# Optimization experiments

Measured on AMD Instinct MI355X. Metric: run time of the kernel, lower is better.

The kernel has to match this reference:

```python
import jax, jax.numpy as jnp
import numpy as np

VEC, H, B, S = 768, 256, 64, 512


def setup_inputs() -> dict:
    key = jax.random.key(0)
    ks = jax.random.split(key, 8)
    sc = 0.02
    return {
        "output_1": jax.random.normal(ks[0], (B, S, VEC), dtype=jnp.float32),
        "output_2": jax.random.normal(ks[1], (B, S, VEC), dtype=jnp.float32),
        "mlp_w": jax.random.normal(ks[2], (H, VEC), dtype=jnp.float32) * sc,
        "mlp_b": jnp.zeros((H,), dtype=jnp.float32),
        "fd_w": jax.random.normal(ks[3], (H, 2 * H), dtype=jnp.float32) * sc,
        "fd_b": jnp.zeros((H,), dtype=jnp.float32),
        "ff_w": jax.random.normal(ks[4], (1, H), dtype=jnp.float32) * sc,
        "ff_b": jnp.zeros((1,), dtype=jnp.float32),
    }


def reference(output_1, output_2, mlp_w, mlp_b, fd_w, fd_b, ff_w, ff_b):
    # eval-mode forward of Bert_coss
    o1 = jax.nn.relu(output_1 @ mlp_w.T + mlp_b)        # [B,S,H]
    o2 = jax.nn.relu(output_2 @ mlp_w.T + mlp_b)        # [B,S,H]
    o1_doc = jnp.mean(o1, axis=1)                        # [B,H]
    o2_doc = jnp.mean(o2, axis=1)                        # [B,H]
    h = jax.nn.relu(jnp.concatenate([o1_doc, o2_doc], axis=1) @ fd_w.T + fd_b)
    out = jax.nn.sigmoid(jnp.squeeze(h @ ff_w.T + ff_b))  # [B]
    # append doc vectors as an extra token
    o1e = jnp.concatenate([o1, o1_doc[:, None, :]], axis=1)  # [B,S+1,H]
    o2e = jnp.concatenate([o2, o2_doc[:, None, :]], axis=1)  # [B,S+1,H]
    # graph_match: scores + softmax over dim=1; only last column is used downstream
    a = jnp.einsum('bsh,bth->bst', o1e, o2e)             # [B,S+1,S+1]
    a_x = jax.nn.softmax(a, axis=1)
    att = a_x[:, :, -1].T                                # [S+1,B]
    att = jnp.concatenate([att[:-1], out[None, :]], axis=0)  # [S+1,B]
    return att
```

## Files before the change

### kernel.cpp

```cpp
#include <hip/hip_runtime.h>
#include <hip/hip_bf16.h>
#include <math.h>

#define B_ 64
#define S_ 512
#define VEC_ 768
#define H_ 256
#define M_ (B_*S_)

typedef float floatx4 __attribute__((ext_vector_type(4)));
typedef __bf16 bf16x8 __attribute__((ext_vector_type(8)));
typedef __bf16 bf16x4 __attribute__((ext_vector_type(4)));

__global__ __launch_bounds__(256) void prep_kernel(
    const float* __restrict__ mlp_w, __bf16* __restrict__ wbf, float* __restrict__ sums)
{
  const int bid = blockIdx.x;
  if (bid < 192) {
    const int i = bid * 256 + threadIdx.x;
    const float4 v = ((const float4*)mlp_w)[i];
    bf16x4 b = { (__bf16)v.x, (__bf16)v.y, (__bf16)v.z, (__bf16)v.w };
    *(bf16x4*)&wbf[(size_t)i * 4] = b;
  } else {
    const int i = (bid - 192) * 256 + threadIdx.x;
    ((float4*)sums)[i] = make_float4(0.f, 0.f, 0.f, 0.f);
  }
}

#define BUFSZ_ 16384
#define LDSB_  32768

__device__ __forceinline__ bf16x8 cvt8(float4 a, float4 b) {
  bf16x8 v;
  v[0] = (__bf16)a.x; v[1] = (__bf16)a.y; v[2] = (__bf16)a.z; v[3] = (__bf16)a.w;
  v[4] = (__bf16)b.x; v[5] = (__bf16)b.y; v[6] = (__bf16)b.z; v[7] = (__bf16)b.w;
  return v;
}

#define LOADT(A0, A1, A2, A3, Bv0, Bv1, kk)                                   \
  {                                                                           \
    const float*  pA_ = Aload + (kk);                                         \
    const __bf16* pB_ = Bload + (kk);                                         \
    A0 = *(const float4*)pA_;                                                 \
    A1 = *(const float4*)(pA_ + 4);                                           \
    A2 = *(const float4*)(pA_ + 64 * VEC_);                                   \
    A3 = *(const float4*)(pA_ + 64 * VEC_ + 4);                               \
    Bv0 = *(const bf16x8*)pB_;                                                \
    Bv1 = *(const bf16x8*)(pB_ + 64 * VEC_);                                  \
  }

#define COMPUTE(bufbase)                                                      \
  {                                                                           \
    bf16x8 af[4], bfr[4];                                                     \
    _Pragma("unroll")                                                         \
    for (int i = 0; i < 4; i++)                                               \
      af[i] = *(const bf16x8*)(smem + (bufbase) + (wm + i * 16 + c) * 64 + aslot); \
    _Pragma("unroll")                                                         \
    for (int j = 0; j < 4; j++)                                               \
      bfr[j] = *(const bf16x8*)(smem + (bufbase) + 8192 + (wn + j * 16 + c) * 64 + aslot); \
    _Pragma("unroll")                                                         \
    for (int i = 0; i < 4; i++)                                               \
      _Pragma("unroll")                                                       \
      for (int j = 0; j < 4; j++)                                             \
        acc[i][j] = __builtin_amdgcn_mfma_f32_16x16x32_bf16(af[i], bfr[j],    \
                                                            acc[i][j], 0, 0, 0); \
  }

#define STEP(A0, A1, A2, A3, Bv0, Bv1, bufbase, kk2, DOLOAD)                  \
  {                                                                           \
    *(bf16x8*)(smem + (bufbase) + woff)               = cvt8(A0, A1);         \
    *(bf16x8*)(smem + (bufbase) + woff + 4096)        = cvt8(A2, A3);         \
    *(bf16x8*)(smem + (bufbase) + 8192 + woff)        = Bv0;                  \
    *(bf16x8*)(smem + (bufbase) + 8192 + woff + 4096) = Bv1;                  \
    if (DOLOAD) { LOADT(A0, A1, A2, A3, Bv0, Bv1, kk2) }                      \
    asm volatile("s_waitcnt lgkmcnt(0)" ::: "memory");                        \
    __builtin_amdgcn_s_barrier();                                             \
    COMPUTE(bufbase);                                                         \
  }

__global__ __launch_bounds__(256, 2) void gemm_doc_kernel(
    const float* __restrict__ out1, const float* __restrict__ out2,
    const __bf16* __restrict__ wbf, const float* __restrict__ mlp_b,
    __bf16* __restrict__ o1, float* __restrict__ sum1, float* __restrict__ sum2)
{
  __shared__ __align__(16) char smem[LDSB_];

  const int tensor = blockIdx.z;
  const float* __restrict__ A = tensor ? out2 : out1;
  float* __restrict__ dsum = tensor ? sum2 : sum1;

  const int n0 = blockIdx.x * 128;
  const int m0 = blockIdx.y * 128;
  const int bidx = m0 >> 9;

  const int t = threadIdx.x;
  const int lane = t & 63;
  const int wave = t >> 6;
  const int q = lane >> 4;
  const int c = lane & 15;
  const int wm = (wave >> 1) * 64;
  const int wn = (wave & 1) * 64;

  const int srow = t >> 2;
  const int woff = srow * 64 + ((((t & 3) ^ (srow & 3) ^ ((srow >> 2) & 3))) << 4);
  const float*  Aload = A   + (size_t)(m0 + srow) * VEC_ + (t & 3) * 8;
  const __bf16* Bload = wbf + (size_t)(n0 + srow) * VEC_ + (t & 3) * 8;

  const int aslot = ((q ^ (c & 3) ^ (c >> 2)) << 4);

  floatx4 acc[4][4];
#pragma unroll
  for (int i = 0; i < 4; i++)
#pragma unroll
    for (int j = 0; j < 4; j++)
      acc[i][j] = (floatx4){0.f, 0.f, 0.f, 0.f};

  float4 a0, a1, a2, a3, e0, e1, e2, e3;
  bf16x8 b0, b1, f0, f1;
  LOADT(a0, a1, a2, a3, b0, b1, 0)
  LOADT(e0, e1, e2, e3, f0, f1, 32)

#pragma unroll 1
  for (int it = 0; it < 11; ++it) {
    STEP(a0, a1, a2, a3, b0, b1, 0,      (2 * it + 2) * 32, 1)
    STEP(e0, e1, e2, e3, f0, f1, BUFSZ_, (2 * it + 3) * 32, 1)
  }
  STEP(a0, a1, a2, a3, b0, b1, 0,      0, 0)
  STEP(e0, e1, e2, e3, f0, f1, BUFSZ_, 0, 0)

#pragma unroll
  for (int j = 0; j < 4; j++) {
    const int n = n0 + wn + j * 16 + c;
    const float bias = mlp_b[n];
    float colsum = 0.f;
#pragma unroll
    for (int i = 0; i < 4; i++) {
      const int mbase = m0 + wm + i * 16 + q * 4;
#pragma unroll
      for (int r = 0; r < 4; r++) {
        float v = acc[i][j][r] + bias;
        v = fmaxf(v, 0.f);
        colsum += v;
        if (tensor == 0) o1[(size_t)(mbase + r) * H_ + n] = (__bf16)v;
      }
    }
    colsum += __shfl_down(colsum, 32);
    colsum += __shfl_down(colsum, 16);
    if (lane < 16)
      atomicAdd(&dsum[bidx * H_ + n0 + wn + j * 16 + lane], colsum);
  }
}

__global__ __launch_bounds__(256) void logits_kernel(
    const __bf16* __restrict__ o1, const float* __restrict__ sum1,
    const float* __restrict__ sum2, float* __restrict__ lg)
{
  const int b = blockIdx.y;
  const int t = threadIdx.x, lane = t & 63, wave = t >> 6;
  const int s = blockIdx.x * 4 + wave;
  if (s > 512) return;
  const float sc = 1.f / 512.f;
  const float4 w4 = ((const float4*)&sum2[b * H_])[lane];
  float p;
  if (s < 512) {
    const bf16x4 x = ((const bf16x4*)&o1[((size_t)b * S_ + s) * H_])[lane];
    p = ((float)x[0] * w4.x + (float)x[1] * w4.y +
         (float)x[2] * w4.z + (float)x[3] * w4.w) * sc;
  } else {
    const float4 x = ((const float4*)&sum1[b * H_])[lane];
    p = (x.x * w4.x + x.y * w4.y + x.z * w4.z + x.w * w4.w) * sc * sc;
  }
  p += __shfl_down(p, 32); p += __shfl_down(p, 16); p += __shfl_down(p, 8);
  p += __shfl_down(p, 4);  p += __shfl_down(p, 2);  p += __shfl_down(p, 1);
  if (lane == 0) lg[b * 513 + s] = p;
}

__global__ __launch_bounds__(256) void softmax_head_kernel(
    const float* __restrict__ lg, const float* __restrict__ sum1, const float* __restrict__ sum2,
    const float* __restrict__ fd_w, const float* __restrict__ fd_b,
    const float* __restrict__ ff_w, const float* __restrict__ ff_b,
    float* __restrict__ out)
{
  const int b = blockIdx.x, t = threadIdx.x, lane = t & 63, wave = t >> 6;
  __shared__ __align__(16) float dc[512];
  __shared__ float sl[513];
  __shared__ float red[4], r1[4], r2[4];

  dc[t]       = sum1[b * H_ + t] * (1.f / 512.f);
  dc[t + 256] = sum2[b * H_ + t] * (1.f / 512.f);
  for (int i = t; i < 513; i += 256) sl[i] = lg[b * 513 + i];
  __syncthreads();
  const float4* wrow = (const float4*)&fd_w[(size_t)t * 512];
  const float4* dc4  = (const float4*)dc;
  float a0 = 0.f, a1 = 0.f;
#pragma unroll 8
  for (int k = 0; k < 128; k += 2) {
    const float4 w0 = wrow[k],     d0 = dc4[k];
    const float4 w1 = wrow[k + 1], d1 = dc4[k + 1];
    a0 += w0.x * d0.x + w0.y * d0.y + w0.z * d0.z + w0.w * d0.w;
    a1 += w1.x * d1.x + w1.y * d1.y + w1.z * d1.z + w1.w * d1.w;
  }
  const float h = fmaxf(a0 + a1 + fd_b[t], 0.f);
  float part = ff_w[t] * h;
  part += __shfl_down(part, 32); part += __shfl_down(part, 16);
  part += __shfl_down(part, 8);  part += __shfl_down(part, 4);
  part += __shfl_down(part, 2);  part += __shfl_down(part, 1);
  if (lane == 0) red[wave] = part;

  float m = -1e30f;
  for (int i = t; i < 513; i += 256) m = fmaxf(m, sl[i]);
  m = fmaxf(m, __shfl_down(m, 32)); m = fmaxf(m, __shfl_down(m, 16));
  m = fmaxf(m, __shfl_down(m, 8));  m = fmaxf(m, __shfl_down(m, 4));
  m = fmaxf(m, __shfl_down(m, 2));  m = fmaxf(m, __shfl_down(m, 1));
  if (lane == 0) r1[wave] = m;
  __syncthreads();
  m = fmaxf(fmaxf(r1[0], r1[1]), fmaxf(r1[2], r1[3]));
  float psum = 0.f;
  for (int i = t; i < 513; i += 256) { const float e = expf(sl[i] - m); sl[i] = e; psum += e; }
  psum += __shfl_down(psum, 32); psum += __shfl_down(psum, 16); psum += __shfl_down(psum, 8);
  psum += __shfl_down(psum, 4);  psum += __shfl_down(psum, 2);  psum += __shfl_down(psum, 1);
  if (lane == 0) r2[wave] = psum;
  __syncthreads();
  const float inv = 1.f / (r2[0] + r2[1] + r2[2] + r2[3]);
  for (int s = t; s < 512; s += 256) out[s * 64 + b] = sl[s] * inv;
  if (t == 0) {
    const float tot = red[0] + red[1] + red[2] + red[3] + ff_b[0];
    out[(size_t)512 * 64 + b] = 1.f / (1.f + expf(-tot));
  }
}

extern "C" void kernel_launch(void* const* d_in, const int* in_sizes, int n_in,
                              void* d_out, int out_size, void* d_ws, size_t ws_size,
                              hipStream_t stream) {
  const float* out1  = (const float*)d_in[0];
  const float* out2  = (const float*)d_in[1];
  const float* mlp_w = (const float*)d_in[2];
  const float* mlp_b = (const float*)d_in[3];
  const float* fd_w  = (const float*)d_in[4];
  const float* fd_b  = (const float*)d_in[5];
  const float* ff_w  = (const float*)d_in[6];
  const float* ff_b  = (const float*)d_in[7];
  float* out = (float*)d_out;

  __bf16* o1  = (__bf16*)d_ws;
  __bf16* wbf = o1 + (size_t)M_ * H_;
  float*  s1  = (float*)(wbf + (size_t)H_ * VEC_);
  float*  s2  = s1 + B_ * H_;
  float*  lgw = s2 + B_ * H_;

  prep_kernel<<<224, 256, 0, stream>>>(mlp_w, wbf, s1);
  gemm_doc_kernel<<<dim3(2, 256, 2), 256, 0, stream>>>(out1, out2, wbf, mlp_b, o1, s1, s2);
  logits_kernel<<<dim3(129, B_), 256, 0, stream>>>(o1, s1, s2, lgw);
  softmax_head_kernel<<<B_, 256, 0, stream>>>(lgw, s1, s2, fd_w, fd_b, ff_w, ff_b, out);
}
```

Before: 292.1 us.

## Widen GEMM K-tile to 128 with a wider swizzled LDS layout

The fp32-input GEMM now stages a 128-wide K slice per iteration instead of 32. Each thread loads 64 floats of A and 64 bf16 of W into registers, and LDS rows are 256 bytes with an XOR swizzle. This cuts the main loop from 24 barrier-separated steps to 6 and keeps more loads in flight per thread. The cost is a 128KB double-buffered LDS footprint, which likely caps the kernel at one block per CU, plus a much larger register staging footprint.

```diff
diff --git a/kernel.cpp b/kernel.cpp
--- a/kernel.cpp
+++ b/kernel.cpp
@@ -27,8 +27,9 @@
   }
 }
 
-#define BUFSZ_ 16384
-#define LDSB_  32768
+#define ABYTES_ 32768
+#define BUFSZ_  65536
+#define LDSB_   131072
 
 __device__ __forceinline__ bf16x8 cvt8(float4 a, float4 b) {
   bf16x8 v;
@@ -37,45 +38,50 @@
   return v;
 }
 
-#define LOADT(A0, A1, A2, A3, Bv0, Bv1, kk)                                   \
+#define LOADT(kk)                                                             \
   {                                                                           \
     const float*  pA_ = Aload + (kk);                                         \
     const __bf16* pB_ = Bload + (kk);                                         \
-    A0 = *(const float4*)pA_;                                                 \
-    A1 = *(const float4*)(pA_ + 4);                                           \
-    A2 = *(const float4*)(pA_ + 64 * VEC_);                                   \
-    A3 = *(const float4*)(pA_ + 64 * VEC_ + 4);                               \
-    Bv0 = *(const bf16x8*)pB_;                                                \
-    Bv1 = *(const bf16x8*)(pB_ + 64 * VEC_);                                  \
+    _Pragma("unroll")                                                         \
+    for (int j_ = 0; j_ < 16; j_++) aR[j_] = *(const float4*)(pA_ + j_ * 4);  \
+    _Pragma("unroll")                                                         \
+    for (int j_ = 0; j_ < 8; j_++)  bR[j_] = *(const bf16x8*)(pB_ + j_ * 8);  \
+  }
+
+#define DSWRITE(bufbase)                                                      \
+  {                                                                           \
+    _Pragma("unroll")                                                         \
+    for (int j_ = 0; j_ < 8; j_++) {                                          \
+      const int phys = (shalf * 8 + j_) ^ (srow & 7);                         \
+      *(bf16x8*)(smem + (bufbase) + srow * 256 + phys * 16) =                 \
+          cvt8(aR[2 * j_], aR[2 * j_ + 1]);                                   \
+    }                                                                         \
+    _Pragma("unroll")                                                         \
+    for (int j_ = 0; j_ < 8; j_++) {                                          \
+      const int phys = (shalf * 8 + j_) ^ (srow & 7);                         \
+      *(bf16x8*)(smem + (bufbase) + ABYTES_ + srow * 256 + phys * 16) = bR[j_]; \
+    }                                                                         \
   }
 
 #define COMPUTE(bufbase)                                                      \
   {                                                                           \
-    bf16x8 af[4], bfr[4];                                                     \
-    _Pragma("unroll")                                                         \
-    for (int i = 0; i < 4; i++)                                               \
-      af[i] = *(const bf16x8*)(smem + (bufbase) + (wm + i * 16 + c) * 64 + aslot); \
-    _Pragma("unroll")                                                         \
-    for (int j = 0; j < 4; j++)                                               \
-      bfr[j] = *(const bf16x8*)(smem + (bufbase) + 8192 + (wn + j * 16 + c) * 64 + aslot); \
-    _Pragma("unroll")                                                         \
-    for (int i = 0; i < 4; i++)                                               \
+    _Pragma("unroll")                                                         \
+    for (int ks = 0; ks < 4; ks++) {                                          \
+      const int slot = ((ks * 4 + q) ^ (c & 7)) * 16;                         \
+      bf16x8 af[4], bfr[4];                                                   \
+      _Pragma("unroll")                                                       \
+      for (int i = 0; i < 4; i++)                                             \
+        af[i] = *(const bf16x8*)(smem + (bufbase) + (wm + i * 16 + c) * 256 + slot); \
       _Pragma("unroll")                                                       \
       for (int j = 0; j < 4; j++)                                             \
-        acc[i][j] = __builtin_amdgcn_mfma_f32_16x16x32_bf16(af[i], bfr[j],    \
-                                                            acc[i][j], 0, 0, 0); \
-  }
-
-#define STEP(A0, A1, A2, A3, Bv0, Bv1, bufbase, kk2, DOLOAD)                  \
-  {                                                                           \
-    *(bf16x8*)(smem + (bufbase) + woff)               = cvt8(A0, A1);         \
-    *(bf16x8*)(smem + (bufbase) + woff + 4096)        = cvt8(A2, A3);         \
-    *(bf16x8*)(smem + (bufbase) + 8192 + woff)        = Bv0;                  \
-    *(bf16x8*)(smem + (bufbase) + 8192 + woff + 4096) = Bv1;                  \
-    if (DOLOAD) { LOADT(A0, A1, A2, A3, Bv0, Bv1, kk2) }                      \
-    asm volatile("s_waitcnt lgkmcnt(0)" ::: "memory");                        \
-    __builtin_amdgcn_s_barrier();                                             \
-    COMPUTE(bufbase);                                                         \
+        bfr[j] = *(const bf16x8*)(smem + (bufbase) + ABYTES_ + (wn + j * 16 + c) * 256 + slot); \
+      _Pragma("unroll")                                                       \
+      for (int i = 0; i < 4; i++)                                             \
+        _Pragma("unroll")                                                     \
+        for (int j = 0; j < 4; j++)                                           \
+          acc[i][j] = __builtin_amdgcn_mfma_f32_16x16x32_bf16(af[i], bfr[j],  \
+                                                              acc[i][j], 0, 0, 0); \
+    }                                                                         \
   }
 
 __global__ __launch_bounds__(256, 2) void gemm_doc_kernel(
@@ -101,12 +107,10 @@
   const int wm = (wave >> 1) * 64;
   const int wn = (wave & 1) * 64;
 
-  const int srow = t >> 2;
-  const int woff = srow * 64 + ((((t & 3) ^ (srow & 3) ^ ((srow >> 2) & 3))) << 4);
-  const float*  Aload = A   + (size_t)(m0 + srow) * VEC_ + (t & 3) * 8;
-  const __bf16* Bload = wbf + (size_t)(n0 + srow) * VEC_ + (t & 3) * 8;
-
-  const int aslot = ((q ^ (c & 3) ^ (c >> 2)) << 4);
+  const int srow  = t >> 1;
+  const int shalf = t & 1;
+  const float*  Aload = A   + (size_t)(m0 + srow) * VEC_ + shalf * 64;
+  const __bf16* Bload = wbf + (size_t)(n0 + srow) * VEC_ + shalf * 64;
 
   floatx4 acc[4][4];
 #pragma unroll
@@ -115,18 +119,21 @@
     for (int j = 0; j < 4; j++)
       acc[i][j] = (floatx4){0.f, 0.f, 0.f, 0.f};
 
-  float4 a0, a1, a2, a3, e0, e1, e2, e3;
-  bf16x8 b0, b1, f0, f1;
-  LOADT(a0, a1, a2, a3, b0, b1, 0)
-  LOADT(e0, e1, e2, e3, f0, f1, 32)
-
+  float4 aR[16];
+  bf16x8 bR[8];
+
+  LOADT(0)
+
+  int bufb = 0;
 #pragma unroll 1
-  for (int it = 0; it < 11; ++it) {
-    STEP(a0, a1, a2, a3, b0, b1, 0,      (2 * it + 2) * 32, 1)
-    STEP(e0, e1, e2, e3, f0, f1, BUFSZ_, (2 * it + 3) * 32, 1)
-  }
-  STEP(a0, a1, a2, a3, b0, b1, 0,      0, 0)
-  STEP(e0, e1, e2, e3, f0, f1, BUFSZ_, 0, 0)
+  for (int kt = 0; kt < 6; ++kt) {
+    DSWRITE(bufb)
+    if (kt < 5) LOADT((kt + 1) * 128)
+    asm volatile("s_waitcnt lgkmcnt(0)" ::: "memory");
+    __builtin_amdgcn_s_barrier();
+    COMPUTE(bufb)
+    bufb ^= BUFSZ_;
+  }
 
 #pragma unroll
   for (int j = 0; j < 4; j++) {
```

After: 313.9 us. 1.07x slower.

## Restructure MLP GEMM to full-N tiles with register-direct A and LDS-staged weights

Applied to the files above, without the earlier changes.

Each block now computes a 128-row by full 256-column tile with 8 waves, loading activations directly from global into registers (triple-buffered) and converting to bf16 in-register, while weight chunks are staged in a double-buffered 128KB swizzled LDS region. This removes the duplicate read of activations across the two N tiles and the A round-trip through LDS. In exchange each wave reads twice as many B fragments from LDS per MFMA, and the large LDS footprint limits occupancy to one block per CU.

```diff
diff --git a/kernel.cpp b/kernel.cpp
--- a/kernel.cpp
+++ b/kernel.cpp
@@ -27,8 +27,7 @@
   }
 }
 
-#define BUFSZ_ 16384
-#define LDSB_  32768
+#define CHUNKB_ 65536
 
 __device__ __forceinline__ bf16x8 cvt8(float4 a, float4 b) {
   bf16x8 v;
@@ -37,117 +36,112 @@
   return v;
 }
 
-#define LOADT(A0, A1, A2, A3, Bv0, Bv1, kk)                                   \
-  {                                                                           \
-    const float*  pA_ = Aload + (kk);                                         \
-    const __bf16* pB_ = Bload + (kk);                                         \
-    A0 = *(const float4*)pA_;                                                 \
-    A1 = *(const float4*)(pA_ + 4);                                           \
-    A2 = *(const float4*)(pA_ + 64 * VEC_);                                   \
-    A3 = *(const float4*)(pA_ + 64 * VEC_ + 4);                               \
-    Bv0 = *(const bf16x8*)pB_;                                                \
-    Bv1 = *(const bf16x8*)(pB_ + 64 * VEC_);                                  \
-  }
-
-#define COMPUTE(bufbase)                                                      \
-  {                                                                           \
-    bf16x8 af[4], bfr[4];                                                     \
-    _Pragma("unroll")                                                         \
-    for (int i = 0; i < 4; i++)                                               \
-      af[i] = *(const bf16x8*)(smem + (bufbase) + (wm + i * 16 + c) * 64 + aslot); \
-    _Pragma("unroll")                                                         \
-    for (int j = 0; j < 4; j++)                                               \
-      bfr[j] = *(const bf16x8*)(smem + (bufbase) + 8192 + (wn + j * 16 + c) * 64 + aslot); \
-    _Pragma("unroll")                                                         \
-    for (int i = 0; i < 4; i++)                                               \
-      _Pragma("unroll")                                                       \
-      for (int j = 0; j < 4; j++)                                             \
-        acc[i][j] = __builtin_amdgcn_mfma_f32_16x16x32_bf16(af[i], bfr[j],    \
-                                                            acc[i][j], 0, 0, 0); \
-  }
-
-#define STEP(A0, A1, A2, A3, Bv0, Bv1, bufbase, kk2, DOLOAD)                  \
-  {                                                                           \
-    *(bf16x8*)(smem + (bufbase) + woff)               = cvt8(A0, A1);         \
-    *(bf16x8*)(smem + (bufbase) + woff + 4096)        = cvt8(A2, A3);         \
-    *(bf16x8*)(smem + (bufbase) + 8192 + woff)        = Bv0;                  \
-    *(bf16x8*)(smem + (bufbase) + 8192 + woff + 4096) = Bv1;                  \
-    if (DOLOAD) { LOADT(A0, A1, A2, A3, Bv0, Bv1, kk2) }                      \
-    asm volatile("s_waitcnt lgkmcnt(0)" ::: "memory");                        \
-    __builtin_amdgcn_s_barrier();                                             \
-    COMPUTE(bufbase);                                                         \
-  }
-
-__global__ __launch_bounds__(256, 2) void gemm_doc_kernel(
+__global__ __launch_bounds__(512, 2) void gemm_doc_kernel(
     const float* __restrict__ out1, const float* __restrict__ out2,
     const __bf16* __restrict__ wbf, const float* __restrict__ mlp_b,
     __bf16* __restrict__ o1, float* __restrict__ sum1, float* __restrict__ sum2)
 {
-  __shared__ __align__(16) char smem[LDSB_];
-
-  const int tensor = blockIdx.z;
+  __shared__ __align__(16) char smem[2 * CHUNKB_];
+
+  const int tensor = blockIdx.y;
   const float* __restrict__ A = tensor ? out2 : out1;
   float* __restrict__ dsum = tensor ? sum2 : sum1;
 
-  const int n0 = blockIdx.x * 128;
-  const int m0 = blockIdx.y * 128;
-  const int bidx = m0 >> 9;
-
+  const int m0 = blockIdx.x * 128;
+  const int bidx = blockIdx.x >> 2;
   const int t = threadIdx.x;
   const int lane = t & 63;
   const int wave = t >> 6;
   const int q = lane >> 4;
   const int c = lane & 15;
-  const int wm = (wave >> 1) * 64;
-  const int wn = (wave & 1) * 64;
-
-  const int srow = t >> 2;
-  const int woff = srow * 64 + ((((t & 3) ^ (srow & 3) ^ ((srow >> 2) & 3))) << 4);
-  const float*  Aload = A   + (size_t)(m0 + srow) * VEC_ + (t & 3) * 8;
-  const __bf16* Bload = wbf + (size_t)(n0 + srow) * VEC_ + (t & 3) * 8;
-
-  const int aslot = ((q ^ (c & 3) ^ (c >> 2)) << 4);
-
-  floatx4 acc[4][4];
+
+  const float* Ap = A + (size_t)(m0 + wave * 16 + c) * VEC_ + q * 8;
+
+  const int brow = t >> 1, bh = t & 1;
+  const __bf16* Bsrc = wbf + (size_t)brow * VEC_ + bh * 64;
+  char* Bdst = smem + brow * 256;
+
+  floatx4 acc[16];
 #pragma unroll
-  for (int i = 0; i < 4; i++)
+  for (int j = 0; j < 16; j++) acc[j] = (floatx4){0.f, 0.f, 0.f, 0.f};
+
+  float4 aR[3][2];
+  bf16x8 sR[8];
+
+#define ALOAD(st) {                                                           \
+    aR[(st) % 3][0] = *(const float4*)(Ap + (st) * 32);                       \
+    aR[(st) % 3][1] = *(const float4*)(Ap + (st) * 32 + 4); }
+
+#define BLOAD(kc) { _Pragma("unroll")                                         \
+    for (int i_ = 0; i_ < 8; i_++)                                            \
+      sR[i_] = *(const bf16x8*)(Bsrc + (kc) * 128 + i_ * 8); }
+
+#define BWRITE(kc) { _Pragma("unroll")                                        \
+    for (int i_ = 0; i_ < 8; i_++)                                            \
+      *(bf16x8*)(Bdst + ((kc) & 1) * CHUNKB_ +                                \
+                 (((bh * 8 + i_) ^ (brow & 7)) * 16)) = sR[i_]; }
+
+#define KSTEP(st) {                                                           \
+    if ((st) + 2 < 24) ALOAD((st) + 2)                                        \
+    const bf16x8 af = cvt8(aR[(st) % 3][0], aR[(st) % 3][1]);                 \
+    const char* bb = smem + (((st) >> 2) & 1) * CHUNKB_ + c * 256 +           \
+                     (((((st) & 3) * 4 + q) ^ (c & 7)) * 16);                 \
+    bf16x8 bfr[8];                                                            \
+    _Pragma("unroll")                                                         \
+    for (int j = 0; j < 8; j++) bfr[j] = *(const bf16x8*)(bb + j * 4096);     \
+    _Pragma("unroll")                                                         \
+    for (int j = 0; j < 8; j++)                                               \
+      acc[j] = __builtin_amdgcn_mfma_f32_16x16x32_bf16(af, bfr[j], acc[j], 0, 0, 0); \
+    _Pragma("unroll")                                                         \
+    for (int j = 0; j < 8; j++) bfr[j] = *(const bf16x8*)(bb + 32768 + j * 4096); \
+    _Pragma("unroll")                                                         \
+    for (int j = 0; j < 8; j++)                                               \
+      acc[8 + j] = __builtin_amdgcn_mfma_f32_16x16x32_bf16(af, bfr[j], acc[8 + j], 0, 0, 0); \
+  }
+
+#define BOUNDARY(cn) {                                                        \
+    BWRITE((cn) + 1)                                                          \
+    if ((cn) < 4) BLOAD((cn) + 2)                                             \
+    asm volatile("s_waitcnt lgkmcnt(0)" ::: "memory");                        \
+    __builtin_amdgcn_s_barrier(); }
+
+  ALOAD(0) ALOAD(1)
+  BLOAD(0)
+  BWRITE(0)
+  BLOAD(1)
+  asm volatile("s_waitcnt lgkmcnt(0)" ::: "memory");
+  __builtin_amdgcn_s_barrier();
+
+  KSTEP(0)  KSTEP(1)  KSTEP(2)  KSTEP(3)  BOUNDARY(0)
+  KSTEP(4)  KSTEP(5)  KSTEP(6)  KSTEP(7)  BOUNDARY(1)
+  KSTEP(8)  KSTEP(9)  KSTEP(10) KSTEP(11) BOUNDARY(2)
+  KSTEP(12) KSTEP(13) KSTEP(14) KSTEP(15) BOUNDARY(3)
+  KSTEP(16) KSTEP(17) KSTEP(18) KSTEP(19) BOUNDARY(4)
+  KSTEP(20) KSTEP(21) KSTEP(22) KSTEP(23)
+
+#undef ALOAD
+#undef BLOAD
+#undef BWRITE
+#undef KSTEP
+#undef BOUNDARY
+
 #pragma unroll
-    for (int j = 0; j < 4; j++)
-      acc[i][j] = (floatx4){0.f, 0.f, 0.f, 0.f};
-
-  float4 a0, a1, a2, a3, e0, e1, e2, e3;
-  bf16x8 b0, b1, f0, f1;
-  LOADT(a0, a1, a2, a3, b0, b1, 0)
-  LOADT(e0, e1, e2, e3, f0, f1, 32)
-
-#pragma unroll 1
-  for (int it = 0; it < 11; ++it) {
-    STEP(a0, a1, a2, a3, b0, b1, 0,      (2 * it + 2) * 32, 1)
-    STEP(e0, e1, e2, e3, f0, f1, BUFSZ_, (2 * it + 3) * 32, 1)
-  }
-  STEP(a0, a1, a2, a3, b0, b1, 0,      0, 0)
-  STEP(e0, e1, e2, e3, f0, f1, BUFSZ_, 0, 0)
-
-#pragma unroll
-  for (int j = 0; j < 4; j++) {
-    const int n = n0 + wn + j * 16 + c;
+  for (int j = 0; j < 16; j++) {
+    const int n = j * 16 + c;
     const float bias = mlp_b[n];
     float colsum = 0.f;
+    const int mb = m0 + wave * 16 + q * 4;
 #pragma unroll
-    for (int i = 0; i < 4; i++) {
-      const int mbase = m0 + wm + i * 16 + q * 4;
-#pragma unroll
-      for (int r = 0; r < 4; r++) {
-        float v = acc[i][j][r] + bias;
-        v = fmaxf(v, 0.f);
-        colsum += v;
-        if (tensor == 0) o1[(size_t)(mbase + r) * H_ + n] = (__bf16)v;
-      }
+    for (int r = 0; r < 4; r++) {
+      float v = acc[j][r] + bias;
+      v = fmaxf(v, 0.f);
+      colsum += v;
+      if (tensor == 0) o1[(size_t)(mb + r) * H_ + n] = (__bf16)v;
     }
     colsum += __shfl_down(colsum, 32);
     colsum += __shfl_down(colsum, 16);
     if (lane < 16)
-      atomicAdd(&dsum[bidx * H_ + n0 + wn + j * 16 + lane], colsum);
+      atomicAdd(&dsum[bidx * H_ + j * 16 + lane], colsum);
   }
 }
 
@@ -249,7 +243,7 @@
   float*  lgw = s2 + B_ * H_;
 
   prep_kernel<<<224, 256, 0, stream>>>(mlp_w, wbf, s1);
-  gemm_doc_kernel<<<dim3(2, 256, 2), 256, 0, stream>>>(out1, out2, wbf, mlp_b, o1, s1, s2);
+  gemm_doc_kernel<<<dim3(256, 2), 512, 0, stream>>>(out1, out2, wbf, mlp_b, o1, s1, s2);
   logits_kernel<<<dim3(129, B_), 256, 0, stream>>>(o1, s1, s2, lgw);
   softmax_head_kernel<<<B_, 256, 0, stream>>>(lgw, s1, s2, fd_w, fd_b, ff_w, ff_b, out);
 }
```

Result: no change. 288.2 us (-1.3%).
